# Kernel tuning notes

Hardware: AMD Instinct MI355X
Metric: run time of the kernel (lower is better)

Reference implementation:

```python
import jax, jax.numpy as jnp
import numpy as np

D_MODEL = 1024
N_HEADS = 16
HEAD_DIM = D_MODEL // N_HEADS
B, S = 4, 2048


def setup_inputs() -> dict:
    key = jax.random.key(0)
    ks = jax.random.split(key, 11)
    scale = 1.0 / np.sqrt(D_MODEL)
    inp = {
        "query": jax.random.normal(ks[0], (B, S, D_MODEL), jnp.float32),
        "key": jax.random.normal(ks[1], (B, S, D_MODEL), jnp.float32),
        "value": jax.random.normal(ks[2], (B, S, D_MODEL), jnp.float32),
        "Wq": jax.random.normal(ks[3], (D_MODEL, D_MODEL), jnp.float32) * scale,
        "bq": jnp.zeros((D_MODEL,), jnp.float32),
        "Wk": jax.random.normal(ks[4], (D_MODEL, D_MODEL), jnp.float32) * scale,
        "bk": jnp.zeros((D_MODEL,), jnp.float32),
        "Wv": jax.random.normal(ks[5], (D_MODEL, D_MODEL), jnp.float32) * scale,
        "bv": jnp.zeros((D_MODEL,), jnp.float32),
        "Wo": jax.random.normal(ks[6], (D_MODEL, D_MODEL), jnp.float32) * scale,
        "bo": jnp.zeros((D_MODEL,), jnp.float32),
    }
    return inp


def _split_heads(x):
    b, s, _ = x.shape
    return x.reshape(b, s, N_HEADS, HEAD_DIM).transpose(0, 2, 1, 3)  # b h s d


def reference(query, key, value, Wq, bq, Wk, bk, Wv, bv, Wo, bo):
    Q = _split_heads(query @ Wq.T + bq)
    K = _split_heads(key @ Wk.T + bk)
    V = _split_heads(value @ Wv.T + bv)
    scale = 1.0 / jnp.sqrt(jnp.float32(HEAD_DIM))
    energy = jnp.einsum("bhqd,bhkd->bhqk", Q, K) * scale  # full N x N scores
    attn = jax.nn.softmax(energy, axis=-1)
    x = jnp.einsum("bhqk,bhkd->bhqd", attn, V)
    x = x.transpose(0, 2, 1, 3).reshape(query.shape[0], -1, D_MODEL)
    return x @ Wo.T + bo
```

## Files before the change

kernel.cpp:

```cpp
#include <hip/hip_runtime.h>
#include <cstdint>
#include <cstddef>


typedef unsigned short u16;
typedef unsigned u32;
typedef short short8 __attribute__((ext_vector_type(8)));
typedef __bf16 bf16x8 __attribute__((ext_vector_type(8)));
typedef float f32x4 __attribute__((ext_vector_type(4)));
typedef float f32x16 __attribute__((ext_vector_type(16)));
typedef unsigned short u16x4 __attribute__((ext_vector_type(4)));
typedef unsigned u32x2 __attribute__((ext_vector_type(2)));
typedef unsigned u32x4 __attribute__((ext_vector_type(4)));
typedef int iv2 __attribute__((ext_vector_type(2)));

__device__ __forceinline__ u16 f2bf(float f) {
  unsigned u = __builtin_bit_cast(unsigned, f);
  u += 0x7fffu + ((u >> 16) & 1u);
  return (u16)(u >> 16);
}
__device__ __forceinline__ bf16x8 bc8(short8 v) { return __builtin_bit_cast(bf16x8, v); }
__device__ __forceinline__ u32 pk_bf16(float a, float b) {
  u32 r;
  asm("v_cvt_pk_bf16_f32 %0, %1, %2" : "=v"(r) : "v"(a), "v"(b));
  return r;
}
__device__ __forceinline__ void gload16(const u16* g, u16* l) {
  __builtin_amdgcn_global_load_lds((const __attribute__((address_space(1))) void*)g,
                                   (__attribute__((address_space(3))) void*)l, 16, 0, 0);
}

__global__ __launch_bounds__(256) void cvt_all(const float* __restrict__ q,
                                               const float* __restrict__ k,
                                               const float* __restrict__ v,
                                               const float* __restrict__ wq,
                                               const float* __restrict__ wk,
                                               const float* __restrict__ wv,
                                               const float* __restrict__ wo,
                                               u16* __restrict__ xq, u16* __restrict__ xk,
                                               u16* __restrict__ xv, u16* __restrict__ wqb,
                                               u16* __restrict__ wkb, u16* __restrict__ wvb,
                                               u16* __restrict__ wob) {
  const size_t i4 = (size_t)blockIdx.x * 256 + threadIdx.x;
  const size_t A4 = 1ull << 21, W4 = 1ull << 18;
  const float* s;
  u16* d;
  size_t off;
  if (i4 < 3 * A4) {
    const int r = (int)(i4 >> 21);
    off = i4 & (A4 - 1);
    s = r == 0 ? q : (r == 1 ? k : v);
    d = r == 0 ? xq : (r == 1 ? xk : xv);
  } else {
    const size_t t = i4 - 3 * A4;
    const int r = (int)(t >> 18);
    off = t & (W4 - 1);
    s = r == 0 ? wq : (r == 1 ? wk : (r == 2 ? wv : wo));
    d = r == 0 ? wqb : (r == 1 ? wkb : (r == 2 ? wvb : wob));
  }
  const f32x4 a = ((const f32x4*)s)[off];
  u32x2 o = {pk_bf16(a[0], a[1]), pk_bf16(a[2], a[3])};
  ((u32x2*)d)[off] = o;
}

__device__ __forceinline__ bf16x8 ldf(const u16* buf, int row, int g) {
  return bc8(*(const short8*)(buf + row * 32 + g * 8));
}

__device__ __forceinline__ void gemm_core(u16* lds, const u16* __restrict__ A,
                                          const u16* __restrict__ Bw,
                                          const float* __restrict__ bias,
                                          void* __restrict__ C, int mode, float oscale) {
  const int t = threadIdx.x;
  const int w = t >> 6, l = t & 63, g = l >> 4, m = l & 15;
  const int wr = w >> 1, wc = w & 1;
  const int m0 = blockIdx.x * 128, n0 = blockIdx.y * 256;
  const u16* gA = A + (size_t)m0 * 1024;
  const u16* gB = Bw + (size_t)n0 * 1024;

  f32x4 acc[4][8];
  const f32x4 z = {0.f, 0.f, 0.f, 0.f};
#pragma unroll
  for (int i = 0; i < 4; ++i)
#pragma unroll
    for (int j = 0; j < 8; ++j) acc[i][j] = z;

#pragma unroll
  for (int tt = 0; tt < 2; ++tt) {
    u16* sA = lds + tt * 12288;
    u16* sB = sA + 4096;
    const int ko = tt * 32;
#pragma unroll
    for (int r = 0; r < 2; ++r) {
      const int c = r * 256 + t;
      gload16(gA + (size_t)(c >> 2) * 1024 + (c & 3) * 8 + ko, sA + c * 8);
    }
#pragma unroll
    for (int r = 0; r < 4; ++r) {
      const int c = r * 256 + t;
      gload16(gB + (size_t)(c >> 2) * 1024 + (c & 3) * 8 + ko, sB + c * 8);
    }
  }
  asm volatile("s_waitcnt vmcnt(6)" ::: "memory");
  __builtin_amdgcn_s_barrier();

  bf16x8 af[4], bfr[8];
  int cb = 0;
  for (int tt = 0; tt < 32; ++tt) {
    u16* bA = lds + cb * 12288;
    u16* bB = bA + 4096;
    const int sbi = (cb == 0) ? 2 : cb - 1;
    u16* sA = lds + sbi * 12288;
    u16* sB = sA + 4096;
    const int ko = (tt + 2) * 32;
    const bool st = tt < 30;

    af[0] = ldf(bA, wr * 64 + m, g);
    af[1] = ldf(bA, wr * 64 + 16 + m, g);
#pragma unroll
    for (int j = 0; j < 4; ++j) bfr[j] = ldf(bB, wc * 128 + j * 16 + m, g);
    if (st) {
#pragma unroll
      for (int r = 0; r < 2; ++r) {
        const int c = r * 256 + t;
        gload16(gA + (size_t)(c >> 2) * 1024 + (c & 3) * 8 + ko, sA + c * 8);
      }
    }
    __builtin_amdgcn_s_barrier();
    __builtin_amdgcn_s_setprio(1);
#pragma unroll
    for (int i = 0; i < 2; ++i)
#pragma unroll
      for (int j = 0; j < 4; ++j)
        acc[i][j] = __builtin_amdgcn_mfma_f32_16x16x32_bf16(af[i], bfr[j], acc[i][j], 0, 0, 0);
    __builtin_amdgcn_s_setprio(0);
    __builtin_amdgcn_s_barrier();

#pragma unroll
    for (int j = 4; j < 8; ++j) bfr[j] = ldf(bB, wc * 128 + j * 16 + m, g);
    if (st) {
#pragma unroll
      for (int r = 0; r < 2; ++r) {
        const int c = r * 256 + t;
        gload16(gB + (size_t)(c >> 2) * 1024 + (c & 3) * 8 + ko, sB + c * 8);
      }
    }
    __builtin_amdgcn_s_barrier();
    __builtin_amdgcn_s_setprio(1);
#pragma unroll
    for (int i = 0; i < 2; ++i)
#pragma unroll
      for (int j = 4; j < 8; ++j)
        acc[i][j] = __builtin_amdgcn_mfma_f32_16x16x32_bf16(af[i], bfr[j], acc[i][j], 0, 0, 0);
    __builtin_amdgcn_s_setprio(0);
    __builtin_amdgcn_s_barrier();

    af[2] = ldf(bA, wr * 64 + 32 + m, g);
    af[3] = ldf(bA, wr * 64 + 48 + m, g);
    if (st) {
#pragma unroll
      for (int r = 2; r < 4; ++r) {
        const int c = r * 256 + t;
        gload16(gB + (size_t)(c >> 2) * 1024 + (c & 3) * 8 + ko, sB + c * 8);
      }
    }
    __builtin_amdgcn_s_barrier();
    __builtin_amdgcn_s_setprio(1);
#pragma unroll
    for (int i = 2; i < 4; ++i)
#pragma unroll
      for (int j = 0; j < 4; ++j)
        acc[i][j] = __builtin_amdgcn_mfma_f32_16x16x32_bf16(af[i], bfr[j], acc[i][j], 0, 0, 0);
    __builtin_amdgcn_s_setprio(0);
    __builtin_amdgcn_s_barrier();

    __builtin_amdgcn_s_setprio(1);
#pragma unroll
    for (int i = 2; i < 4; ++i)
#pragma unroll
      for (int j = 4; j < 8; ++j)
        acc[i][j] = __builtin_amdgcn_mfma_f32_16x16x32_bf16(af[i], bfr[j], acc[i][j], 0, 0, 0);
    __builtin_amdgcn_s_setprio(0);
    if (tt < 30)
      asm volatile("s_waitcnt vmcnt(6)" ::: "memory");
    else
      asm volatile("s_waitcnt vmcnt(0)" ::: "memory");
    __builtin_amdgcn_s_barrier();
    cb = (cb == 2) ? 0 : cb + 1;
  }

  float bv[8];
#pragma unroll
  for (int j = 0; j < 8; ++j) bv[j] = bias[n0 + wc * 128 + j * 16 + m];

  if (mode == 2) {
#pragma unroll
    for (int i = 0; i < 4; ++i)
#pragma unroll
      for (int j = 0; j < 8; ++j) {
        const int row0 = m0 + wr * 64 + i * 16 + g * 4;
        const int col = n0 + wc * 128 + j * 16 + m;
        u16x4 o;
#pragma unroll
        for (int r = 0; r < 4; ++r) o[r] = f2bf((acc[i][j][r] + bv[j]) * oscale);
        *(u16x4*)((u16*)C + ((size_t)(row0 >> 11) * 1024 + col) * 2048 + (row0 & 2047)) = o;
      }
  } else {
#pragma unroll
    for (int i = 0; i < 4; ++i) {
#pragma unroll
      for (int r = 0; r < 4; ++r) {
        const int row = m0 + wr * 64 + i * 16 + g * 4 + r;
#pragma unroll
        for (int j = 0; j < 8; ++j) {
          const int col = n0 + wc * 128 + j * 16 + m;
          const float v = (acc[i][j][r] + bv[j]) * oscale;
          if (mode == 0)
            ((float*)C)[(size_t)row * 1024 + col] = v;
          else
            ((u16*)C)[(size_t)row * 1024 + col] = f2bf(v);
        }
      }
    }
  }
}

__global__ __launch_bounds__(256, 2) void qkv_gemm(const u16* __restrict__ xq,
                                                   const u16* __restrict__ xk,
                                                   const u16* __restrict__ xv,
                                                   const u16* __restrict__ wqb,
                                                   const u16* __restrict__ wkb,
                                                   const u16* __restrict__ wvb,
                                                   const float* __restrict__ bq,
                                                   const float* __restrict__ bk,
                                                   const float* __restrict__ bv,
                                                   u16* __restrict__ Qp, u16* __restrict__ Kp,
                                                   u16* __restrict__ Vt, float SC) {
  __shared__ alignas(16) u16 lds[36864];
  const int z = blockIdx.z;
  const u16* A = z == 0 ? xq : (z == 1 ? xk : xv);
  const u16* W = z == 0 ? wqb : (z == 1 ? wkb : wvb);
  const float* bi = z == 0 ? bq : (z == 1 ? bk : bv);
  void* C = z == 0 ? (void*)Qp : (z == 1 ? (void*)Kp : (void*)Vt);
  gemm_core(lds, A, W, bi, C, z == 2 ? 2 : 1, z == 0 ? SC : 1.f);
}

__global__ __launch_bounds__(256, 2) void o_gemm(const u16* __restrict__ Xa,
                                                 const u16* __restrict__ wob,
                                                 const float* __restrict__ bo,
                                                 float* __restrict__ out) {
  __shared__ alignas(16) u16 lds[36864];
  gemm_core(lds, Xa, wob, bo, out, 0, 1.f);
}

__global__ __launch_bounds__(256, 2) void attn_fwd(const u16* __restrict__ Q,
                                                   const u16* __restrict__ Kp,
                                                   const u16* __restrict__ Vt,
                                                   u16* __restrict__ Xa) {
  __shared__ alignas(16) u16 kl[2][64][72];
  __shared__ alignas(16) u16 vl[2][64][72];
  const int tid = threadIdx.x;
  const int l = tid & 63, w = tid >> 6;
  const int q32 = l & 31, hi = l >> 5;
  const int lin = blockIdx.x + 8 * blockIdx.y;
  const int xp = lin >> 6, yp = lin & 63;
  const int b = yp >> 4, h = yp & 15;
  const int q0 = xp * 256 + w * 64;

  bf16x8 qf[2][4];
  const size_t qrow = (size_t)b * 2048 + q0 + q32;
#pragma unroll
  for (int qg = 0; qg < 2; ++qg)
#pragma unroll
    for (int ds = 0; ds < 4; ++ds)
      qf[qg][ds] = bc8(*(const short8*)(Q + (qrow + qg * 32) * 1024 + h * 64 + ds * 16 + hi * 8));

  f32x16 of[2][2] = {{{}, {}}, {{}, {}}};
  float ls[2][4] = {{0.f, 0.f, 0.f, 0.f}, {0.f, 0.f, 0.f, 0.f}};

  const int sr = tid >> 3;
  const int sc8 = (tid & 7) * 8;
  const u16* Kb = Kp + (size_t)b * 2048 * 1024 + h * 64;
  const u16* Vb = Vt + (size_t)yp * 64 * 2048;

  short8 rk[2], rv[2];
#pragma unroll
  for (int it = 0; it < 2; ++it) {
    const int r = sr + it * 32;
    rk[it] = *(const short8*)(Kb + (size_t)r * 1024 + sc8);
    rv[it] = *(const short8*)(Vb + (size_t)r * 2048 + sc8);
    *(short8*)(&kl[0][r][sc8]) = rk[it];
    *(short8*)(&vl[0][r][sc8]) = rv[it];
  }
#pragma unroll
  for (int it = 0; it < 2; ++it) {
    const int r = sr + it * 32;
    rk[it] = *(const short8*)(Kb + (size_t)(64 + r) * 1024 + sc8);
    rv[it] = *(const short8*)(Vb + (size_t)r * 2048 + 64 + sc8);
  }
  asm volatile("s_waitcnt lgkmcnt(0)\n\ts_barrier" ::: "memory");

  for (int kt = 0; kt < 32; ++kt) {
    const int cur = kt & 1;

#pragma unroll
    for (int kt2 = 0; kt2 < 2; ++kt2) {
      bf16x8 kf[4];
#pragma unroll
      for (int ds = 0; ds < 4; ++ds)
        kf[ds] = bc8(*(const short8*)(&kl[cur][kt2 * 32 + q32][ds * 16 + hi * 8]));
      f32x16 st[2];
      __builtin_amdgcn_s_setprio(1);
#pragma unroll
      for (int qg = 0; qg < 2; ++qg) {
        f32x16 s = {};
#pragma unroll
        for (int ds = 0; ds < 4; ++ds)
          s = __builtin_amdgcn_mfma_f32_32x32x16_bf16(kf[ds], qf[qg][ds], s, 0, 0, 0);
        st[qg] = s;
      }
      __builtin_amdgcn_s_setprio(0);

      if (kt2 == 0) {
        if (kt + 1 < 32) {
#pragma unroll
          for (int it = 0; it < 2; ++it) {
            const int r = sr + it * 32;
            *(short8*)(&kl[cur ^ 1][r][sc8]) = rk[it];
            *(short8*)(&vl[cur ^ 1][r][sc8]) = rv[it];
          }
        }
        if (kt + 2 < 32) {
#pragma unroll
          for (int it = 0; it < 2; ++it) {
            const int r = sr + it * 32;
            rk[it] = *(const short8*)(Kb + (size_t)((kt + 2) * 64 + r) * 1024 + sc8);
            rv[it] = *(const short8*)(Vb + (size_t)r * 2048 + (kt + 2) * 64 + sc8);
          }
        }
      }

      bf16x8 pbf[2][2];
#pragma unroll
      for (int qg = 0; qg < 2; ++qg) {
        float p[16];
#pragma unroll
        for (int r = 0; r < 16; ++r) p[r] = __builtin_amdgcn_exp2f(st[qg][r]);
        ls[qg][0] += (p[0] + p[1]) + (p[2] + p[3]);
        ls[qg][1] += (p[4] + p[5]) + (p[6] + p[7]);
        ls[qg][2] += (p[8] + p[9]) + (p[10] + p[11]);
        ls[qg][3] += (p[12] + p[13]) + (p[14] + p[15]);
#pragma unroll
        for (int s = 0; s < 2; ++s) {
          int X0 = (int)pk_bf16(p[8 * s + 0], p[8 * s + 1]);
          int X1 = (int)pk_bf16(p[8 * s + 2], p[8 * s + 3]);
          int Y0 = (int)pk_bf16(p[8 * s + 4], p[8 * s + 5]);
          int Y1 = (int)pk_bf16(p[8 * s + 6], p[8 * s + 7]);
          iv2 r0 = __builtin_amdgcn_permlane32_swap(X0, Y0, false, false);
          iv2 r1 = __builtin_amdgcn_permlane32_swap(X1, Y1, false, false);
          u32x4 bw = {(u32)r0[0], (u32)r1[0], (u32)r0[1], (u32)r1[1]};
          pbf[qg][s] = __builtin_bit_cast(bf16x8, bw);
        }
      }

#pragma unroll
      for (int s = 0; s < 2; ++s) {
        const int ks = kt2 * 2 + s;
        __builtin_amdgcn_s_setprio(1);
#pragma unroll
        for (int dt = 0; dt < 2; ++dt) {
          const bf16x8 vf = bc8(*(const short8*)(&vl[cur][dt * 32 + q32][ks * 16 + hi * 8]));
#pragma unroll
          for (int qg = 0; qg < 2; ++qg)
            of[qg][dt] = __builtin_amdgcn_mfma_f32_32x32x16_bf16(vf, pbf[qg][s], of[qg][dt], 0, 0, 0);
        }
        __builtin_amdgcn_s_setprio(0);
      }
    }
    asm volatile("s_waitcnt lgkmcnt(0)\n\ts_barrier" ::: "memory");
  }

#pragma unroll
  for (int qg = 0; qg < 2; ++qg) {
    float lo = (ls[qg][0] + ls[qg][1]) + (ls[qg][2] + ls[qg][3]);
    lo += __shfl_xor(lo, 32, 64);
    const float inv = 1.0f / lo;
    const size_t qr = qrow + qg * 32;
#pragma unroll
    for (int dt = 0; dt < 2; ++dt)
#pragma unroll
      for (int rg = 0; rg < 4; ++rg) {
        u32x2 o2;
        o2[0] = pk_bf16(of[qg][dt][4 * rg + 0] * inv, of[qg][dt][4 * rg + 1] * inv);
        o2[1] = pk_bf16(of[qg][dt][4 * rg + 2] * inv, of[qg][dt][4 * rg + 3] * inv);
        *(u32x2*)(Xa + qr * 1024 + h * 64 + dt * 32 + rg * 8 + hi * 4) = o2;
      }
  }
}

extern "C" void kernel_launch(void* const* d_in, const int* in_sizes, int n_in,
                              void* d_out, int out_size, void* d_ws, size_t ws_size,
                              hipStream_t stream) {
  const float* q  = (const float*)d_in[0];
  const float* k  = (const float*)d_in[1];
  const float* v  = (const float*)d_in[2];
  const float* Wq = (const float*)d_in[3];
  const float* bq = (const float*)d_in[4];
  const float* Wk = (const float*)d_in[5];
  const float* bk = (const float*)d_in[6];
  const float* Wv = (const float*)d_in[7];
  const float* bv = (const float*)d_in[8];
  const float* Wo = (const float*)d_in[9];
  const float* bo = (const float*)d_in[10];

  char* ws = (char*)d_ws;
  const size_t MB = 1024ull * 1024ull;
  u16* wqb = (u16*)(ws + 0 * MB);
  u16* wkb = (u16*)(ws + 2 * MB);
  u16* wvb = (u16*)(ws + 4 * MB);
  u16* wob = (u16*)(ws + 6 * MB);
  u16* xq  = (u16*)(ws + 8 * MB);
  u16* xk  = (u16*)(ws + 24 * MB);
  u16* xv  = (u16*)(ws + 40 * MB);
  u16* Qp  = (u16*)(ws + 56 * MB);
  u16* Kp  = (u16*)(ws + 72 * MB);
  u16* Vt  = (u16*)(ws + 88 * MB);
  u16* Xa  = xq;

  cvt_all<<<28672, 256, 0, stream>>>(q, k, v, Wq, Wk, Wv, Wo,
                                     xq, xk, xv, wqb, wkb, wvb, wob);

  const float SC = 0.125f * 1.44269504f;
  qkv_gemm<<<dim3(64, 4, 3), 256, 0, stream>>>(xq, xk, xv, wqb, wkb, wvb,
                                               bq, bk, bv, Qp, Kp, Vt, SC);

  attn_fwd<<<dim3(8, 64), 256, 0, stream>>>(Qp, Kp, Vt, Xa);

  o_gemm<<<dim3(64, 4), 256, 0, stream>>>(Xa, wob, bo, (float*)d_out);
}
```

Before: 195.0 us.

## Software-pipeline QK^T one tile ahead with triple-buffered K/V LDS

Moves K/V shared memory from double to triple buffering and computes the next tile's QK^T scores during the current tile's softmax and PV phase. The goal is to let the MFMA score work overlap the exp2/pack VALU work. Prefetch depth grows by one tile, with global loads issued three tiles ahead. In exchange, LDS use rises by half, and keeping both scores and outputs live raises register pressure, which may hurt occupancy under the launch bound of 2.

```diff
diff --git a/kernel.cpp b/kernel.cpp
--- a/kernel.cpp
+++ b/kernel.cpp
@@ -257,8 +257,8 @@
                                                    const u16* __restrict__ Kp,
                                                    const u16* __restrict__ Vt,
                                                    u16* __restrict__ Xa) {
-  __shared__ alignas(16) u16 kl[2][64][72];
-  __shared__ alignas(16) u16 vl[2][64][72];
+  __shared__ alignas(16) u16 kl[3][64][72];
+  __shared__ alignas(16) u16 vl[3][64][72];
   const int tid = threadIdx.x;
   const int l = tid & 63, w = tid >> 6;
   const int q32 = l & 31, hi = l >> 5;
@@ -285,67 +285,54 @@
 
   short8 rk[2], rv[2];
 #pragma unroll
+  for (int tt = 0; tt < 2; ++tt) {
+#pragma unroll
+    for (int it = 0; it < 2; ++it) {
+      const int r = sr + it * 32;
+      rk[it] = *(const short8*)(Kb + (size_t)(tt * 64 + r) * 1024 + sc8);
+      rv[it] = *(const short8*)(Vb + (size_t)r * 2048 + tt * 64 + sc8);
+      *(short8*)(&kl[tt][r][sc8]) = rk[it];
+      *(short8*)(&vl[tt][r][sc8]) = rv[it];
+    }
+  }
+#pragma unroll
   for (int it = 0; it < 2; ++it) {
     const int r = sr + it * 32;
-    rk[it] = *(const short8*)(Kb + (size_t)r * 1024 + sc8);
-    rv[it] = *(const short8*)(Vb + (size_t)r * 2048 + sc8);
-    *(short8*)(&kl[0][r][sc8]) = rk[it];
-    *(short8*)(&vl[0][r][sc8]) = rv[it];
-  }
-#pragma unroll
-  for (int it = 0; it < 2; ++it) {
-    const int r = sr + it * 32;
-    rk[it] = *(const short8*)(Kb + (size_t)(64 + r) * 1024 + sc8);
-    rv[it] = *(const short8*)(Vb + (size_t)r * 2048 + 64 + sc8);
+    rk[it] = *(const short8*)(Kb + (size_t)(128 + r) * 1024 + sc8);
+    rv[it] = *(const short8*)(Vb + (size_t)r * 2048 + 128 + sc8);
   }
   asm volatile("s_waitcnt lgkmcnt(0)\n\ts_barrier" ::: "memory");
 
+  f32x16 st[2][2];
+#pragma unroll
+  for (int kt2 = 0; kt2 < 2; ++kt2) {
+    bf16x8 kf[4];
+#pragma unroll
+    for (int ds = 0; ds < 4; ++ds)
+      kf[ds] = bc8(*(const short8*)(&kl[0][kt2 * 32 + q32][ds * 16 + hi * 8]));
+#pragma unroll
+    for (int qg = 0; qg < 2; ++qg) {
+      f32x16 s = {};
+#pragma unroll
+      for (int ds = 0; ds < 4; ++ds)
+        s = __builtin_amdgcn_mfma_f32_32x32x16_bf16(kf[ds], qf[qg][ds], s, 0, 0, 0);
+      st[kt2][qg] = s;
+    }
+  }
+
+  int cb = 0;
   for (int kt = 0; kt < 32; ++kt) {
-    const int cur = kt & 1;
+    const int nx = (cb == 2) ? 0 : cb + 1;
+    const int sb = (nx == 2) ? 0 : nx + 1;
 
 #pragma unroll
     for (int kt2 = 0; kt2 < 2; ++kt2) {
-      bf16x8 kf[4];
-#pragma unroll
-      for (int ds = 0; ds < 4; ++ds)
-        kf[ds] = bc8(*(const short8*)(&kl[cur][kt2 * 32 + q32][ds * 16 + hi * 8]));
-      f32x16 st[2];
-      __builtin_amdgcn_s_setprio(1);
-#pragma unroll
-      for (int qg = 0; qg < 2; ++qg) {
-        f32x16 s = {};
-#pragma unroll
-        for (int ds = 0; ds < 4; ++ds)
-          s = __builtin_amdgcn_mfma_f32_32x32x16_bf16(kf[ds], qf[qg][ds], s, 0, 0, 0);
-        st[qg] = s;
-      }
-      __builtin_amdgcn_s_setprio(0);
-
-      if (kt2 == 0) {
-        if (kt + 1 < 32) {
-#pragma unroll
-          for (int it = 0; it < 2; ++it) {
-            const int r = sr + it * 32;
-            *(short8*)(&kl[cur ^ 1][r][sc8]) = rk[it];
-            *(short8*)(&vl[cur ^ 1][r][sc8]) = rv[it];
-          }
-        }
-        if (kt + 2 < 32) {
-#pragma unroll
-          for (int it = 0; it < 2; ++it) {
-            const int r = sr + it * 32;
-            rk[it] = *(const short8*)(Kb + (size_t)((kt + 2) * 64 + r) * 1024 + sc8);
-            rv[it] = *(const short8*)(Vb + (size_t)r * 2048 + (kt + 2) * 64 + sc8);
-          }
-        }
-      }
-
       bf16x8 pbf[2][2];
 #pragma unroll
       for (int qg = 0; qg < 2; ++qg) {
         float p[16];
 #pragma unroll
-        for (int r = 0; r < 16; ++r) p[r] = __builtin_amdgcn_exp2f(st[qg][r]);
+        for (int r = 0; r < 16; ++r) p[r] = __builtin_amdgcn_exp2f(st[kt2][qg][r]);
         ls[qg][0] += (p[0] + p[1]) + (p[2] + p[3]);
         ls[qg][1] += (p[4] + p[5]) + (p[6] + p[7]);
         ls[qg][2] += (p[8] + p[9]) + (p[10] + p[11]);
@@ -363,13 +350,49 @@
         }
       }
 
+      if (kt + 1 < 32) {
+        bf16x8 kf[4];
+#pragma unroll
+        for (int ds = 0; ds < 4; ++ds)
+          kf[ds] = bc8(*(const short8*)(&kl[nx][kt2 * 32 + q32][ds * 16 + hi * 8]));
+        __builtin_amdgcn_s_setprio(1);
+#pragma unroll
+        for (int qg = 0; qg < 2; ++qg) {
+          f32x16 s = {};
+#pragma unroll
+          for (int ds = 0; ds < 4; ++ds)
+            s = __builtin_amdgcn_mfma_f32_32x32x16_bf16(kf[ds], qf[qg][ds], s, 0, 0, 0);
+          st[kt2][qg] = s;
+        }
+        __builtin_amdgcn_s_setprio(0);
+      }
+
+      if (kt2 == 0) {
+        if (kt + 2 < 32) {
+#pragma unroll
+          for (int it = 0; it < 2; ++it) {
+            const int r = sr + it * 32;
+            *(short8*)(&kl[sb][r][sc8]) = rk[it];
+            *(short8*)(&vl[sb][r][sc8]) = rv[it];
+          }
+        }
+        if (kt + 3 < 32) {
+#pragma unroll
+          for (int it = 0; it < 2; ++it) {
+            const int r = sr + it * 32;
+            rk[it] = *(const short8*)(Kb + (size_t)((kt + 3) * 64 + r) * 1024 + sc8);
+            rv[it] = *(const short8*)(Vb + (size_t)r * 2048 + (kt + 3) * 64 + sc8);
+          }
+        }
+      }
+
 #pragma unroll
       for (int s = 0; s < 2; ++s) {
         const int ks = kt2 * 2 + s;
         __builtin_amdgcn_s_setprio(1);
 #pragma unroll
         for (int dt = 0; dt < 2; ++dt) {
-          const bf16x8 vf = bc8(*(const short8*)(&vl[cur][dt * 32 + q32][ks * 16 + hi * 8]));
+          const bf16x8 vf = bc8(*(const short8*)(&vl[cb][dt * 32 + q32][ks * 16 + hi * 8]));
 #pragma unroll
           for (int qg = 0; qg < 2; ++qg)
             of[qg][dt] = __builtin_amdgcn_mfma_f32_32x32x16_bf16(vf, pbf[qg][s], of[qg][dt], 0, 0, 0);
@@ -378,6 +401,7 @@
       }
     }
     asm volatile("s_waitcnt lgkmcnt(0)\n\ts_barrier" ::: "memory");
+    cb = nx;
   }
 
 #pragma unroll
```

Measured after the change: 196.4 us. No clear change (+0.7%).
